# Kernel tuning notes

Hardware: AMD Instinct MI355X
Metric: run time of the kernel (lower is better)

Reference implementation:

```python
import jax, jax.numpy as jnp
import numpy as np

WS = 8      # window size
SS = 4      # shift size
NH = 4      # num heads
EPS = 1e-5
MLP_RATIO = 4


def _win_part(x, ws):
    # x: [B,D,H,W,C] -> [B*nD*nH*nW, ws^3, C]
    B, D, H, W, C = x.shape
    x = x.reshape(B, D // ws, ws, H // ws, ws, W // ws, ws, C)
    x = x.transpose(0, 1, 3, 5, 2, 4, 6, 7)
    return x.reshape(-1, ws * ws * ws, C)


def _win_rev(w, ws, B, D, H, W):
    C = w.shape[-1]
    x = w.reshape(B, D // ws, H // ws, W // ws, ws, ws, ws, C)
    x = x.transpose(0, 1, 4, 2, 5, 3, 6, 7)
    return x.reshape(B, D, H, W, C)


def _ln(x, g, b):
    m = jnp.mean(x, axis=-1, keepdims=True)
    v = jnp.mean((x - m) ** 2, axis=-1, keepdims=True)
    return (x - m) / jnp.sqrt(v + EPS) * g + b


def _rel_index(ws):
    coords = np.stack(np.meshgrid(np.arange(ws), np.arange(ws), np.arange(ws), indexing='ij'))  # [3,ws,ws,ws]
    cf = coords.reshape(3, -1)                      # [3, ws^3]
    rel = (cf[:, :, None] - cf[:, None, :]).transpose(1, 2, 0) + (ws - 1)  # [N,N,3]
    return rel[..., 0] * (2 * ws - 1) ** 2 + rel[..., 1] * (2 * ws - 1) + rel[..., 2]


def _attn_mask(D, H, W, ws, ss):
    img = np.zeros((1, D, H, W, 1), dtype=np.float32)
    cnt = 0
    sl = (slice(0, -ws), slice(-ws, -ss), slice(-ss, None))
    for d in sl:
        for h in sl:
            for w in sl:
                img[:, d, h, w, :] = cnt
                cnt += 1
    mw = np.asarray(_win_part(jnp.asarray(img), ws))[..., 0]  # [nW, ws^3]
    diff = mw[:, None, :] - mw[:, :, None]
    return np.where(diff != 0, -100.0, 0.0).astype(np.float32)


def setup_inputs() -> dict:
    key = jax.random.key(0)
    ks = jax.random.split(key, 12)
    B, D, H, W, C = 1, 16, 64, 64, 128
    mh = MLP_RATIO * C
    s = 0.02
    return {
        'x': jax.random.normal(ks[0], (B, D, H, W, C), jnp.float32),
        'attn_mask': jnp.asarray(_attn_mask(D, H, W, WS, SS)),
        'rel_index': jnp.asarray(_rel_index(WS), jnp.int32),
        'rel_bias': jax.random.normal(ks[1], ((2 * WS - 1) ** 3, NH), jnp.float32) * s,
        'qkv_w': jax.random.normal(ks[2], (3 * C, C), jnp.float32) * s,
        'qkv_b': jnp.zeros((3 * C,), jnp.float32),
        'proj_w': jax.random.normal(ks[3], (C, C), jnp.float32) * s,
        'proj_b': jnp.zeros((C,), jnp.float32),
        'norm1_g': jnp.ones((C,), jnp.float32),
        'norm1_b': jnp.zeros((C,), jnp.float32),
        'norm2_g': jnp.ones((C,), jnp.float32),
        'norm2_b': jnp.zeros((C,), jnp.float32),
        'mlp_w1': jax.random.normal(ks[4], (mh, C), jnp.float32) * s,
        'mlp_b1': jnp.zeros((mh,), jnp.float32),
        'mlp_w2': jax.random.normal(ks[5], (C, mh), jnp.float32) * s,
        'mlp_b2': jnp.zeros((C,), jnp.float32),
    }


def reference(x, attn_mask, rel_index, rel_bias, qkv_w, qkv_b, proj_w, proj_b,
              norm1_g, norm1_b, norm2_g, norm2_b, mlp_w1, mlp_b1, mlp_w2, mlp_b2):
    B, D, H, W, C = x.shape
    ws, ss, nh = WS, SS, NH
    hd = C // nh
    scale = hd ** -0.5
    N = ws ** 3
    shortcut = x
    h = _ln(x, norm1_g, norm1_b)
    h = jnp.roll(h, (-ss, -ss, -ss), axis=(1, 2, 3))
    xw = _win_part(h, ws)                 # [B_, N, C]
    B_ = xw.shape[0]
    nW = attn_mask.shape[0]
    qkv = xw @ qkv_w.T + qkv_b            # [B_, N, 3C]
    qkv = qkv.reshape(B_, N, 3, nh, hd).transpose(2, 0, 3, 1, 4)  # [3,B_,h,N,hd]
    q, k, v = qkv[0] * scale, qkv[1], qkv[2]
    attn = jnp.einsum('bhnd,bhmd->bhnm', q, k)
    rpe = rel_bias[rel_index.reshape(-1)].reshape(N, N, nh).transpose(2, 0, 1)  # [h,N,N]
    attn = attn + rpe[None]
    attn = attn.reshape(B_ // nW, nW, nh, N, N) + attn_mask[None, :, None]
    attn = jax.nn.softmax(attn.reshape(B_, nh, N, N), axis=-1)
    out = jnp.einsum('bhnm,bhmd->bhnd', attn, v).transpose(0, 2, 1, 3).reshape(B_, N, C)
    out = out @ proj_w.T + proj_b
    out = _win_rev(out, ws, B, D, H, W)
    out = jnp.roll(out, (ss, ss, ss), axis=(1, 2, 3))
    x = shortcut + out
    h2 = _ln(x, norm2_g, norm2_b)
    h2 = jax.nn.gelu(h2 @ mlp_w1.T + mlp_b1, approximate=False)
    return x + h2 @ mlp_w2.T + mlp_b2
```

## Files before the change

kernel.cpp:

```cpp
#include <hip/hip_runtime.h>
#include <math.h>

typedef __bf16 bf16;
typedef __bf16 bf16x4 __attribute__((ext_vector_type(4)));
typedef __bf16 bf16x8 __attribute__((ext_vector_type(8)));
typedef float f32x4 __attribute__((ext_vector_type(4)));
typedef unsigned short u16;
typedef u16 u16x2 __attribute__((ext_vector_type(2)));

#define LOG2E 1.4426950408889634f

__device__ __forceinline__ float b2f(u16 b) {
  return (float)__builtin_bit_cast(bf16, b);
}

__global__ void sniff_k(const unsigned* __restrict__ xw_, int* __restrict__ flag) {
  int lane = threadIdx.x;
  int c = 0;
#pragma unroll
  for (int j = 0; j < 4; j++) {
    unsigned e = (xw_[lane * 4 + j] >> 7) & 0xFFu;
    c += (e >= 100u && e <= 140u) ? 1 : 0;
  }
#pragma unroll
  for (int d = 1; d < 64; d <<= 1) c += __shfl_xor(c, d);
  if (lane == 0) *flag = (c >= 150) ? 1 : 0;
}

__global__ __launch_bounds__(256) void canon_norm_k(
    const void* __restrict__ sg, const void* __restrict__ sb,
    bf16* __restrict__ dg, bf16* __restrict__ db, const int* __restrict__ flag) {
  int i = threadIdx.x;
  int fl = *flag;
  if (i < 128) {
    dg[i] = fl ? ((const bf16*)sg)[i] : (bf16)((const float*)sg)[i];
  } else {
    int j = i - 128;
    db[j] = fl ? ((const bf16*)sb)[j] : (bf16)((const float*)sb)[j];
  }
}

struct ProArgs {
  const int* ridx;
  const void* rbias;
  bf16* rpem;
  const void* x;
  const bf16* g1;
  const bf16* b1n;
  bf16* xw;
  const void* csrc[12];
  bf16* cdst[12];
  int cn[12];
};

__global__ __launch_bounds__(256) void pro_k(ProArgs a,
                                             const int* __restrict__ flag) {
  const int bx = blockIdx.x, tid = threadIdx.x;
  const int fl = *flag;
  if (bx < 8192) {
    int t = bx * 256 + tid;
    int m0 = (t & 127) * 4, q = (t >> 7) & 511, h = (t >> 16) & 3, ty = t >> 18;
    int qd = q >> 6, qh = (q >> 3) & 7, qw = q & 7;
    int kt = m0 >> 6, mt = (m0 >> 4) & 3, quad = (m0 >> 2) & 3;
    int4 ri = *(const int4*)&a.ridx[q * 512 + m0];
    const int rv[4] = {ri.x, ri.y, ri.z, ri.w};
    bf16x4 o;
#pragma unroll
    for (int j = 0; j < 4; j++) {
      int m = m0 + j;
      int md = m >> 6, mh = (m >> 3) & 7, mw = m & 7;
      bool diff = ((ty & 4) && ((qd < 4) != (md < 4))) ||
                  ((ty & 2) && ((qh < 4) != (mh < 4))) ||
                  ((ty & 1) && ((qw < 4) != (mw < 4)));
      float bv = fl ? (float)((const bf16*)a.rbias)[rv[j] * 4 + h]
                    : ((const float*)a.rbias)[rv[j] * 4 + h];
      float v = bv * LOG2E;
      o[j] = (bf16)(v + (diff ? -144.2695041f : 0.f));
    }
    size_t out = ((size_t)(ty * 4 + h) << 18) +
                 (((size_t)(kt * 4 + quad) * 512 + q) * 16 + mt * 4);
    *(bf16x4*)&a.rpem[out] = o;
  } else if (bx < 24576) {
    int wave = tid >> 6, lane = tid & 63;
    int tok = (bx - 8192) * 4 + wave;
    int win = tok >> 9, pos = tok & 511;
    int rd = (win >> 6) * 8 + (pos >> 6);
    int rh = ((win >> 3) & 7) * 8 + ((pos >> 3) & 7);
    int rw = (win & 7) * 8 + (pos & 7);
    int od = (rd + 4) & 15, oh = (rh + 4) & 63, ow = (rw + 4) & 63;
    size_t src = (size_t)((od * 64 + oh) * 64 + ow) * 128;
    int ch = lane * 2;
    float f0, f1;
    if (!fl) {
      const float* xf = (const float*)a.x + src + ch;
      f0 = xf[0];
      f1 = xf[1];
    } else {
      u16x2 xv = *(const u16x2*)((const bf16*)a.x + src + ch);
      f0 = b2f(xv[0]);
      f1 = b2f(xv[1]);
    }
    float s = f0 + f1, sq = f0 * f0 + f1 * f1;
#pragma unroll
    for (int d = 1; d < 64; d <<= 1) {
      s += __shfl_xor(s, d);
      sq += __shfl_xor(sq, d);
    }
    float mean = s * (1.f / 128.f);
    float var = sq * (1.f / 128.f) - mean * mean;
    float rstd = rsqrtf(fmaxf(var, 0.f) + 1e-5f);
    u16x2 gv = *(const u16x2*)(a.g1 + ch), bv = *(const u16x2*)(a.b1n + ch);
    u16x2 ov;
    ov[0] =
        __builtin_bit_cast(u16, (bf16)((f0 - mean) * rstd * b2f(gv[0]) + b2f(bv[0])));
    ov[1] =
        __builtin_bit_cast(u16, (bf16)((f1 - mean) * rstd * b2f(gv[1]) + b2f(bv[1])));
    *(u16x2*)(a.xw + (size_t)tok * 128 + ch) = ov;
  } else {
    int seg = bx - 24576;
    int ti = seg >> 8;
    int i = (seg & 255) * 256 + tid;
    if (i < a.cn[ti]) {
      if (fl)
        a.cdst[ti][i] = ((const bf16*)a.csrc[ti])[i];
      else
        a.cdst[ti][i] = (bf16)((const float*)a.csrc[ti])[i];
    }
  }
}

template <int EPI, int BM, int BK, int N_, int K_>
__global__ __launch_bounds__(256) void gemm_k(const bf16* __restrict__ A,
                                              const bf16* __restrict__ B,
                                              const bf16* __restrict__ bias,
                                              void* __restrict__ outv,
                                              const void* __restrict__ residv,
                                              const int* __restrict__ flag) {
  constexpr int NC = K_ / BK;
  constexpr int NBUF = (NC > 1) ? 2 : 1;
  __shared__ __align__(16) u16 SM[NBUF][(BM + 128) * BK];
  const int t = threadIdx.x;
  const int wave = t >> 6, lane = t & 63, l15 = lane & 15, quad = lane >> 4;
  const int m0 = blockIdx.x * BM, n0 = blockIdx.y * 128;
  constexpr int MI = BM / 32;
  int fl = 0;
  if constexpr (EPI == 1) fl = *flag;
  f32x4 acc[MI][4] = {};
  const int wr = (wave >> 1) * (BM / 2), wc = (wave & 1) * 64;
  constexpr int TPR = BK / 8;
  constexpr int RPP = 256 / TPR;
  constexpr int PASSES = (BM + 128) / RPP;
  const int srow = t / TPR, sc16 = t % TPR;

  auto stage = [&](int c, int buf) {
#pragma unroll
    for (int p = 0; p < PASSES; p++) {
      int row = p * RPP + srow;
      int cs = sc16 ^ (row & 7);
      const u16* src;
      if (row < BM)
        src = (const u16*)A + (size_t)(m0 + row) * K_ + c * BK + cs * 8;
      else
        src = (const u16*)B + (size_t)(n0 + row - BM) * K_ + c * BK + cs * 8;
      __builtin_amdgcn_global_load_lds(
          (const __attribute__((address_space(1))) void*)src,
          (__attribute__((address_space(3))) void*)&SM[buf][row * BK + sc16 * 8],
          16, 0, 0);
    }
  };

  stage(0, 0);
  __syncthreads();
#pragma unroll
  for (int c = 0; c < NC; c++) {
    if (c + 1 < NC) stage(c + 1, (c + 1) & 1);
    const char* cur = (const char*)SM[c & 1];
#pragma unroll
    for (int ks = 0; ks < BK / 32; ks++) {
      bf16x8 a[MI], b[4];
#pragma unroll
      for (int i = 0; i < MI; i++) {
        int row = wr + i * 16 + l15;
        a[i] = *(const bf16x8*)(cur + row * (BK * 2) +
                                (((ks * 4 + quad) ^ (row & 7)) << 4));
      }
#pragma unroll
      for (int j = 0; j < 4; j++) {
        int row = BM + wc + j * 16 + l15;
        b[j] = *(const bf16x8*)(cur + row * (BK * 2) +
                                (((ks * 4 + quad) ^ (row & 7)) << 4));
      }
#pragma unroll
      for (int i = 0; i < MI; i++)
#pragma unroll
        for (int j = 0; j < 4; j++)
          acc[i][j] =
              __builtin_amdgcn_mfma_f32_16x16x32_bf16(a[i], b[j], acc[i][j], 0, 0, 0);
    }
    if (c + 1 < NC) __syncthreads();
  }
  const float qscale = 0.17677669529663687f * LOG2E;
#pragma unroll
  for (int i = 0; i < MI; i++) {
#pragma unroll
    for (int r = 0; r < 4; r++) {
      int tok = m0 + wr + i * 16 + quad * 4 + r;
      size_t obase = 0;
      if constexpr (EPI == 1) {
        int win = tok >> 9, pos = tok & 511;
        int rd = (win >> 6) * 8 + (pos >> 6);
        int rh = ((win >> 3) & 7) * 8 + ((pos >> 3) & 7);
        int rw = (win & 7) * 8 + (pos & 7);
        int od = (rd + 4) & 15, oh = (rh + 4) & 63, ow = (rw + 4) & 63;
        obase = (size_t)((od * 64 + oh) * 64 + ow) * 128;
      }
#pragma unroll
      for (int j = 0; j < 4; j++) {
        int gn = n0 + wc + j * 16 + l15;
        float v = acc[i][j][r] + (float)bias[gn];
        if constexpr (EPI == 0) {
          int tensor = gn >> 7, c = gn & 127, head = c >> 5, d = c & 31;
          if (tensor == 0) v *= qscale;
          int win = tok >> 9, pos = tok & 511;
          size_t off = ((((size_t)tensor * 4 + head) * 128 + win) * 512 + pos) * 32 + d;
          ((bf16*)outv)[off] = (bf16)v;
        } else {
          float rs = fl ? (float)((const bf16*)residv)[obase + gn]
                        : ((const float*)residv)[obase + gn];
          v += rs;
          ((bf16*)outv)[obase + gn] = (bf16)v;
        }
      }
    }
  }
}

__global__ __launch_bounds__(256) void mlp_k(const bf16* __restrict__ X2,
                                             const bf16* __restrict__ G2,
                                             const bf16* __restrict__ B2n,
                                             const bf16* __restrict__ W1,
                                             const bf16* __restrict__ B1,
                                             const bf16* __restrict__ W2,
                                             const bf16* __restrict__ B2,
                                             void* __restrict__ outv,
                                             const int* __restrict__ flag) {
  __shared__ __align__(16) u16 sA[32 * 128];
  __shared__ __align__(16) u16 sB[128 * 128];
  __shared__ __align__(16) u16 sH[32 * 520];
  const int t = threadIdx.x;
  const int wave = t >> 6, lane = t & 63, l15 = lane & 15, quad = lane >> 4;
  const int m0 = blockIdx.x * 32;
  const int wr = (wave >> 1) * 16, wc = (wave & 1) * 64;
  const int fl = *flag;
  const int srow = t >> 4, sc16 = t & 15;

  auto stage_w = [&](const bf16* W, int chunk, int wK) {
#pragma unroll
    for (int p = 0; p < 8; p++) {
      int row = p * 16 + srow;
      int cs = sc16 ^ (row & 7);
      const u16* src = (const u16*)W +
                       (size_t)(wK == 128 ? (chunk * 128 + row) : row) * wK +
                       (wK == 128 ? 0 : chunk * 128) + cs * 8;
      __builtin_amdgcn_global_load_lds(
          (const __attribute__((address_space(1))) void*)src,
          (__attribute__((address_space(3))) void*)&sB[row * 128 + sc16 * 8], 16,
          0, 0);
    }
  };

  {
#pragma unroll
    for (int p = 0; p < 2; p++) {
      int row = p * 16 + srow;
      int cs = sc16 ^ (row & 7);
      __builtin_amdgcn_global_load_lds(
          (const __attribute__((address_space(1))) void*)((const u16*)X2 +
                                                          (size_t)(m0 + row) * 128 +
                                                          cs * 8),
          (__attribute__((address_space(3))) void*)&sA[row * 128 + sc16 * 8], 16,
          0, 0);
    }
  }
  stage_w(W1, 0, 128);
  __syncthreads();

  {
    int r = t >> 3, k = t & 7;
    bf16x8 c0 = *(const bf16x8*)&sA[r * 128 + (k * 2 + 0) * 8];
    bf16x8 c1 = *(const bf16x8*)&sA[r * 128 + (k * 2 + 1) * 8];
    float s = 0.f, sq = 0.f;
#pragma unroll
    for (int e = 0; e < 8; e++) {
      float f0 = (float)c0[e], f1 = (float)c1[e];
      s += f0 + f1;
      sq += f0 * f0 + f1 * f1;
    }
#pragma unroll
    for (int d = 1; d < 8; d <<= 1) {
      s += __shfl_xor(s, d);
      sq += __shfl_xor(sq, d);
    }
    float mean = s * (1.f / 128.f);
    float var = sq * (1.f / 128.f) - mean * mean;
    float rstd = rsqrtf(fmaxf(var, 0.f) + 1e-5f);
    __syncthreads();
#pragma unroll
    for (int j = 0; j < 2; j++) {
      int tc = ((k * 2 + j) ^ (r & 7)) * 8;
      bf16x8 gv = *(const bf16x8*)&G2[tc];
      bf16x8 bv = *(const bf16x8*)&B2n[tc];
      bf16x8 cv = j ? c1 : c0;
      bf16x8 ov;
#pragma unroll
      for (int e = 0; e < 8; e++)
        ov[e] = (bf16)(((float)cv[e] - mean) * rstd * (float)gv[e] + (float)bv[e]);
      *(bf16x8*)&sA[r * 128 + (k * 2 + j) * 8] = ov;
    }
  }
  __syncthreads();

#pragma unroll 1
  for (int nc = 0; nc < 4; nc++) {
    f32x4 acc1[4] = {};
#pragma unroll
    for (int ks = 0; ks < 4; ks++) {
      int arow = wr + l15;
      bf16x8 av = *(const bf16x8*)((const char*)sA + arow * 256 +
                                   (((ks * 4 + quad) ^ (arow & 7)) << 4));
      bf16x8 bv[4];
#pragma unroll
      for (int j = 0; j < 4; j++) {
        int row = wc + j * 16 + l15;
        bv[j] = *(const bf16x8*)((const char*)sB + row * 256 +
                                 (((ks * 4 + quad) ^ (row & 7)) << 4));
      }
#pragma unroll
      for (int j = 0; j < 4; j++)
        acc1[j] = __builtin_amdgcn_mfma_f32_16x16x32_bf16(av, bv[j], acc1[j], 0, 0, 0);
    }
#pragma unroll
    for (int j = 0; j < 4; j++) {
      int ncol = nc * 128 + wc + j * 16 + l15;
      float bj = (float)B1[ncol];
#pragma unroll
      for (int r = 0; r < 4; r++) {
        float v = acc1[j][r] + bj;
        float v2 = v * v;
        float u2 = v * (2.30220806f + 0.10294323f * v2);
        float e2 = exp2f(u2);
        v = v - v * __builtin_amdgcn_rcpf(e2 + 1.f);
        sH[(wr + quad * 4 + r) * 520 + ncol] = __builtin_bit_cast(u16, (bf16)v);
      }
    }
    __syncthreads();
    if (nc < 3)
      stage_w(W1, nc + 1, 128);
    else
      stage_w(W2, 0, 512);
    __syncthreads();
  }

  f32x4 acc2[4] = {};
#pragma unroll 1
  for (int kc = 0; kc < 4; kc++) {
#pragma unroll
    for (int ks = 0; ks < 4; ks++) {
      int arow = wr + l15;
      bf16x8 av = *(const bf16x8*)((const char*)sH + arow * 1040 +
                                   (kc * 128 + ks * 32 + quad * 8) * 2);
#pragma unroll
      for (int j = 0; j < 4; j++) {
        int row = wc + j * 16 + l15;
        bf16x8 bv = *(const bf16x8*)((const char*)sB + row * 256 +
                                     (((ks * 4 + quad) ^ (row & 7)) << 4));
        acc2[j] = __builtin_amdgcn_mfma_f32_16x16x32_bf16(av, bv, acc2[j], 0, 0, 0);
      }
    }
    if (kc < 3) {
      __syncthreads();
      stage_w(W2, kc + 1, 512);
      __syncthreads();
    }
  }
#pragma unroll
  for (int j = 0; j < 4; j++) {
    int gn = wc + j * 16 + l15;
    float bj = (float)B2[gn];
#pragma unroll
    for (int r = 0; r < 4; r++) {
      int tok = m0 + wr + quad * 4 + r;
      size_t off = (size_t)tok * 128 + gn;
      float v = acc2[j][r] + bj + (float)X2[off];
      if (fl)
        ((bf16*)outv)[off] = (bf16)v;
      else
        ((float*)outv)[off] = v;
    }
  }
}

__global__ __launch_bounds__(512, 4) void attn_k(const bf16* __restrict__ qkv,
                                                 const bf16* __restrict__ rpem,
                                                 bf16* __restrict__ att) {
  __shared__ __align__(16) bf16 sVt[32 * 512];
  __shared__ __align__(16) bf16 sP[8][32 * 64];
  const int t = threadIdx.x;
  const int p = blockIdx.x;
  const int win = ((p >> 6) << 3) | (p & 7);
  const int mid = (p >> 3) & 7;
  const int head = mid >> 1, qh = mid & 1;
  const int wave = t >> 6, lane = t & 63, l15 = lane & 15, quad = lane >> 4;

  const int wd = win >> 6, wh = (win >> 3) & 7, ww = win & 7;
  const int type = ((wd == 1) << 2) | ((wh == 7) << 1) | (ww == 7);

  const size_t hw32 = (size_t)512 * 32;
  const bf16* qp = qkv + ((size_t)(0 * 4 + head) * 128 + win) * hw32;
  const bf16* kp = qkv + ((size_t)(1 * 4 + head) * 128 + win) * hw32;
  const bf16* vp = qkv + ((size_t)(2 * 4 + head) * 128 + win) * hw32;
  const bf16* rpeh = rpem + ((size_t)(type * 4 + head) << 18);
  const int qbase = qh * 256 + wave * 32;

  {
    int kpi = t >> 3, dblk = (t & 7) * 4;
    char* sb = (char*)sVt;
#pragma unroll
    for (int kb = 0; kb < 4; kb++) {
      const bf16* v0 = vp + (size_t)(kb * 128 + 2 * kpi) * 32 + dblk;
      bf16x4 a = *(const bf16x4*)v0;
      bf16x4 b = *(const bf16x4*)(v0 + 32);
      int keyw = kb * 64 + kpi;
#pragma unroll
      for (int dd = 0; dd < 4; dd++) {
        int row = dblk + dd;
        unsigned wv = (unsigned)__builtin_bit_cast(u16, a[dd]) |
                      ((unsigned)__builtin_bit_cast(u16, b[dd]) << 16);
        *(unsigned*)(sb + ((row * 1024 + keyw * 4) ^ ((row & 7) << 4))) = wv;
      }
    }
  }

  bf16x8 qa[2];
#pragma unroll
  for (int nt = 0; nt < 2; nt++)
    qa[nt] = *(const bf16x8*)(qp + (size_t)(qbase + nt * 16 + l15) * 32 + quad * 8);

  bf16x8 ones;
#pragma unroll
  for (int e = 0; e < 8; e++) ones[e] = (bf16)1.0f;

  __syncthreads();

  f32x4 O[2][2] = {};
  f32x4 O2[2] = {};
  char* pw = (char*)sP[wave];
  const char* sv = (const char*)sVt;
  const int swz = (l15 & 7) << 4;

#pragma unroll 1
  for (int kt = 0; kt < 8; kt++) {
    bf16x8 kb[4];
    bf16x8 rv8[2][2];
#pragma unroll
    for (int mt = 0; mt < 4; mt++)
      kb[mt] = *(const bf16x8*)(kp + (size_t)(kt * 64 + mt * 16 + l15) * 32 +
                                quad * 8);
#pragma unroll
    for (int nt = 0; nt < 2; nt++) {
      const bf16* rb =
          rpeh + ((size_t)(kt * 4 + quad) * 512 + (qbase + nt * 16 + l15)) * 16;
      rv8[nt][0] = *(const bf16x8*)rb;
      rv8[nt][1] = *(const bf16x8*)(rb + 8);
    }
    f32x4 S[4][2];
#pragma unroll
    for (int mt = 0; mt < 4; mt++)
#pragma unroll
      for (int nt = 0; nt < 2; nt++) {
        f32x4 c;
#pragma unroll
        for (int r = 0; r < 4; r++) c[r] = (float)rv8[nt][mt >> 1][(mt & 1) * 4 + r];
        S[mt][nt] = __builtin_amdgcn_mfma_f32_16x16x32_bf16(kb[mt], qa[nt], c, 0, 0, 0);
      }
#pragma unroll
    for (int nt = 0; nt < 2; nt++)
#pragma unroll
      for (int mt = 0; mt < 4; mt++) {
        bf16x4 pv;
#pragma unroll
        for (int r = 0; r < 4; r++) pv[r] = (bf16)exp2f(S[mt][nt][r]);
        *(bf16x4*)(pw + (((nt * 16 + l15) * 128 + mt * 32 + quad * 8) ^ swz)) = pv;
      }
#pragma unroll
    for (int s = 0; s < 2; s++) {
      int vc = kt * 128 + s * 64 + quad * 16;
      int pc = s * 64 + quad * 16;
      bf16x8 va0 = *(const bf16x8*)(sv + ((l15 * 1024 + vc) ^ swz));
      bf16x8 va1 = *(const bf16x8*)(sv + (((16 + l15) * 1024 + vc) ^ swz));
      bf16x8 pb0 = *(const bf16x8*)(pw + ((l15 * 128 + pc) ^ swz));
      bf16x8 pb1 = *(const bf16x8*)(pw + (((16 + l15) * 128 + pc) ^ swz));
      O[0][0] = __builtin_amdgcn_mfma_f32_16x16x32_bf16(va0, pb0, O[0][0], 0, 0, 0);
      O[0][1] = __builtin_amdgcn_mfma_f32_16x16x32_bf16(va0, pb1, O[0][1], 0, 0, 0);
      O[1][0] = __builtin_amdgcn_mfma_f32_16x16x32_bf16(va1, pb0, O[1][0], 0, 0, 0);
      O[1][1] = __builtin_amdgcn_mfma_f32_16x16x32_bf16(va1, pb1, O[1][1], 0, 0, 0);
      O2[0] = __builtin_amdgcn_mfma_f32_16x16x32_bf16(ones, pb0, O2[0], 0, 0, 0);
      O2[1] = __builtin_amdgcn_mfma_f32_16x16x32_bf16(ones, pb1, O2[1], 0, 0, 0);
    }
  }
#pragma unroll
  for (int nt = 0; nt < 2; nt++) {
    float inv = __builtin_amdgcn_rcpf(O2[nt][0]);
    int q = qbase + nt * 16 + l15;
#pragma unroll
    for (int dm = 0; dm < 2; dm++) {
      bf16x4 o;
#pragma unroll
      for (int r = 0; r < 4; r++) o[r] = (bf16)(O[dm][nt][r] * inv);
      *(bf16x4*)(att + ((size_t)win * 512 + q) * 128 + head * 32 + dm * 16 +
                 quad * 4) = o;
    }
  }
}

extern "C" void kernel_launch(void* const* d_in, const int* in_sizes, int n_in,
                              void* d_out, int out_size, void* d_ws,
                              size_t ws_size, hipStream_t stream) {
  const int* rel_index = (const int*)d_in[2];
  char* w = (char*)d_ws;

  int* flag = (int*)w;
  bf16* qw_c = (bf16*)(w + (128ull << 10));
  bf16* pw_c = (bf16*)(w + (256ull << 10));
  bf16* w1_c = (bf16*)(w + (320ull << 10));
  bf16* w2_c = (bf16*)(w + (512ull << 10));
  bf16* qb_c = (bf16*)(w + (704ull << 10));
  bf16* pb_c = (bf16*)(w + (708ull << 10));
  bf16* g1_c = (bf16*)(w + (712ull << 10));
  bf16* b1n_c = (bf16*)(w + (716ull << 10));
  bf16* g2_c = (bf16*)(w + (720ull << 10));
  bf16* b2n_c = (bf16*)(w + (724ull << 10));
  bf16* mb1_c = (bf16*)(w + (728ull << 10));
  bf16* mb2_c = (bf16*)(w + (732ull << 10));
  bf16* xw = (bf16*)(w + (17ull << 20));
  bf16* qkvb = (bf16*)(w + (33ull << 20));
  bf16* x2 = (bf16*)(w + (99ull << 20));
  bf16* rpem = x2;
  bf16* att = xw;

  sniff_k<<<1, 64, 0, stream>>>((const unsigned*)d_in[0], flag);
  canon_norm_k<<<1, 256, 0, stream>>>(d_in[8], d_in[9], g1_c, b1n_c, flag);

  ProArgs pa;
  pa.ridx = rel_index;
  pa.rbias = d_in[3];
  pa.rpem = rpem;
  pa.x = d_in[0];
  pa.g1 = g1_c;
  pa.b1n = b1n_c;
  pa.xw = xw;
  const int srcidx[12] = {4, 5, 6, 7, 8, 9, 10, 11, 12, 13, 14, 15};
  bf16* dsts[12] = {qw_c, qb_c, pw_c, pb_c, g1_c, b1n_c,
                    g2_c, b2n_c, w1_c, mb1_c, w2_c, mb2_c};
  for (int i = 0; i < 12; i++) {
    pa.csrc[i] = d_in[srcidx[i]];
    pa.cdst[i] = dsts[i];
    pa.cn[i] = in_sizes[srcidx[i]];
  }
  pro_k<<<27648, 256, 0, stream>>>(pa, flag);

  gemm_k<0, 32, 128, 384, 128><<<dim3(2048, 3), 256, 0, stream>>>(
      xw, qw_c, qb_c, qkvb, nullptr, flag);
  attn_k<<<1024, 512, 0, stream>>>(qkvb, rpem, att);
  gemm_k<1, 32, 128, 128, 128><<<dim3(2048, 1), 256, 0, stream>>>(
      att, pw_c, pb_c, x2, d_in[0], flag);
  mlp_k<<<2048, 256, 0, stream>>>(x2, g2_c, b2n_c, w1_c, mb1_c, w2_c, mb2_c,
                                  d_out, flag);
}
```

Baseline: 376.8 us.

## Prefetch MLP weights into registers and merge attention query halves per block

In the MLP kernel, the next weight chunk is now loaded from global memory into registers before the current chunk's MFMA work and written to LDS afterwards, replacing direct global-to-LDS loads issued after the barrier. The aim is to hide weight-fetch latency behind compute, at the cost of extra VGPRs. In the attention kernel, each block now handles both query halves of a window-head in a loop, halving the grid to 512 blocks. This reuses the V tile staged in LDS across both halves but reduces parallelism.

```diff
diff --git a/kernel.cpp b/kernel.cpp
--- a/kernel.cpp
+++ b/kernel.cpp
@@ -254,21 +254,6 @@
   const int fl = *flag;
   const int srow = t >> 4, sc16 = t & 15;
 
-  auto stage_w = [&](const bf16* W, int chunk, int wK) {
-#pragma unroll
-    for (int p = 0; p < 8; p++) {
-      int row = p * 16 + srow;
-      int cs = sc16 ^ (row & 7);
-      const u16* src = (const u16*)W +
-                       (size_t)(wK == 128 ? (chunk * 128 + row) : row) * wK +
-                       (wK == 128 ? 0 : chunk * 128) + cs * 8;
-      __builtin_amdgcn_global_load_lds(
-          (const __attribute__((address_space(1))) void*)src,
-          (__attribute__((address_space(3))) void*)&sB[row * 128 + sc16 * 8], 16,
-          0, 0);
-    }
-  };
-
   {
 #pragma unroll
     for (int p = 0; p < 2; p++) {
@@ -281,8 +266,18 @@
           (__attribute__((address_space(3))) void*)&sA[row * 128 + sc16 * 8], 16,
           0, 0);
     }
-  }
-  stage_w(W1, 0, 128);
+#pragma unroll
+    for (int p = 0; p < 8; p++) {
+      int row = p * 16 + srow;
+      int cs = sc16 ^ (row & 7);
+      __builtin_amdgcn_global_load_lds(
+          (const __attribute__((address_space(1))) void*)((const u16*)W1 +
+                                                          (size_t)row * 128 +
+                                                          cs * 8),
+          (__attribute__((address_space(3))) void*)&sB[row * 128 + sc16 * 8], 16,
+          0, 0);
+    }
+  }
   __syncthreads();
 
   {
@@ -320,8 +315,24 @@
   }
   __syncthreads();
 
+  bf16x8 wreg[8];
+
 #pragma unroll 1
   for (int nc = 0; nc < 4; nc++) {
+    {
+      const bf16* Wn = (nc < 3) ? W1 : W2;
+      const int chunk = (nc < 3) ? nc + 1 : 0;
+      const int wK = (nc < 3) ? 128 : 512;
+#pragma unroll
+      for (int p = 0; p < 8; p++) {
+        int row = p * 16 + srow;
+        int cs = sc16 ^ (row & 7);
+        const u16* src = (const u16*)Wn +
+                         (size_t)(wK == 128 ? (chunk * 128 + row) : row) * wK +
+                         (wK == 128 ? 0 : chunk * 128) + cs * 8;
+        wreg[p] = *(const bf16x8*)src;
+      }
+    }
     f32x4 acc1[4] = {};
 #pragma unroll
     for (int ks = 0; ks < 4; ks++) {
@@ -354,16 +365,28 @@
       }
     }
     __syncthreads();
-    if (nc < 3)
-      stage_w(W1, nc + 1, 128);
-    else
-      stage_w(W2, 0, 512);
+#pragma unroll
+    for (int p = 0; p < 8; p++) {
+      int row = p * 16 + srow;
+      *(bf16x8*)&sB[row * 128 + sc16 * 8] = wreg[p];
+    }
     __syncthreads();
   }
 
   f32x4 acc2[4] = {};
 #pragma unroll 1
   for (int kc = 0; kc < 4; kc++) {
+    if (kc < 3) {
+      const int chunk = kc + 1;
+#pragma unroll
+      for (int p = 0; p < 8; p++) {
+        int row = p * 16 + srow;
+        int cs = sc16 ^ (row & 7);
+        const u16* src =
+            (const u16*)W2 + (size_t)row * 512 + chunk * 128 + cs * 8;
+        wreg[p] = *(const bf16x8*)src;
+      }
+    }
 #pragma unroll
     for (int ks = 0; ks < 4; ks++) {
       int arow = wr + l15;
@@ -379,7 +402,11 @@
     }
     if (kc < 3) {
       __syncthreads();
-      stage_w(W2, kc + 1, 512);
+#pragma unroll
+      for (int p = 0; p < 8; p++) {
+        int row = p * 16 + srow;
+        *(bf16x8*)&sB[row * 128 + sc16 * 8] = wreg[p];
+      }
       __syncthreads();
     }
   }
@@ -407,9 +434,8 @@
   __shared__ __align__(16) bf16 sP[8][32 * 64];
   const int t = threadIdx.x;
   const int p = blockIdx.x;
-  const int win = ((p >> 6) << 3) | (p & 7);
-  const int mid = (p >> 3) & 7;
-  const int head = mid >> 1, qh = mid & 1;
+  const int win = ((p >> 5) << 3) | (p & 7);
+  const int head = (p >> 3) & 3;
   const int wave = t >> 6, lane = t & 63, l15 = lane & 15, quad = lane >> 4;
 
   const int wd = win >> 6, wh = (win >> 3) & 7, ww = win & 7;
@@ -420,7 +446,6 @@
   const bf16* kp = qkv + ((size_t)(1 * 4 + head) * 128 + win) * hw32;
   const bf16* vp = qkv + ((size_t)(2 * 4 + head) * 128 + win) * hw32;
   const bf16* rpeh = rpem + ((size_t)(type * 4 + head) << 18);
-  const int qbase = qh * 256 + wave * 32;
 
   {
     int kpi = t >> 3, dblk = (t & 7) * 4;
@@ -441,84 +466,93 @@
     }
   }
 
-  bf16x8 qa[2];
-#pragma unroll
-  for (int nt = 0; nt < 2; nt++)
-    qa[nt] = *(const bf16x8*)(qp + (size_t)(qbase + nt * 16 + l15) * 32 + quad * 8);
-
   bf16x8 ones;
 #pragma unroll
   for (int e = 0; e < 8; e++) ones[e] = (bf16)1.0f;
 
   __syncthreads();
 
-  f32x4 O[2][2] = {};
-  f32x4 O2[2] = {};
   char* pw = (char*)sP[wave];
   const char* sv = (const char*)sVt;
   const int swz = (l15 & 7) << 4;
 
 #pragma unroll 1
-  for (int kt = 0; kt < 8; kt++) {
-    bf16x8 kb[4];
-    bf16x8 rv8[2][2];
-#pragma unroll
-    for (int mt = 0; mt < 4; mt++)
-      kb[mt] = *(const bf16x8*)(kp + (size_t)(kt * 64 + mt * 16 + l15) * 32 +
-                                quad * 8);
+  for (int qh = 0; qh < 2; qh++) {
+    const int qbase = qh * 256 + wave * 32;
+    bf16x8 qa[2];
+#pragma unroll
+    for (int nt = 0; nt < 2; nt++)
+      qa[nt] =
+          *(const bf16x8*)(qp + (size_t)(qbase + nt * 16 + l15) * 32 + quad * 8);
+
+    f32x4 O[2][2] = {};
+    f32x4 O2[2] = {};
+
+#pragma unroll 1
+    for (int kt = 0; kt < 8; kt++) {
+      bf16x8 kb[4];
+      bf16x8 rv8[2][2];
+#pragma unroll
+      for (int mt = 0; mt < 4; mt++)
+        kb[mt] = *(const bf16x8*)(kp + (size_t)(kt * 64 + mt * 16 + l15) * 32 +
+                                  quad * 8);
+#pragma unroll
+      for (int nt = 0; nt < 2; nt++) {
+        const bf16* rb =
+            rpeh + ((size_t)(kt * 4 + quad) * 512 + (qbase + nt * 16 + l15)) * 16;
+        rv8[nt][0] = *(const bf16x8*)rb;
+        rv8[nt][1] = *(const bf16x8*)(rb + 8);
+      }
+      f32x4 S[4][2];
+#pragma unroll
+      for (int mt = 0; mt < 4; mt++)
+#pragma unroll
+        for (int nt = 0; nt < 2; nt++) {
+          f32x4 c;
+#pragma unroll
+          for (int r = 0; r < 4; r++)
+            c[r] = (float)rv8[nt][mt >> 1][(mt & 1) * 4 + r];
+          S[mt][nt] =
+              __builtin_amdgcn_mfma_f32_16x16x32_bf16(kb[mt], qa[nt], c, 0, 0, 0);
+        }
+#pragma unroll
+      for (int nt = 0; nt < 2; nt++)
+#pragma unroll
+        for (int mt = 0; mt < 4; mt++) {
+          bf16x4 pv;
+#pragma unroll
+          for (int r = 0; r < 4; r++) pv[r] = (bf16)exp2f(S[mt][nt][r]);
+          *(bf16x4*)(pw + (((nt * 16 + l15) * 128 + mt * 32 + quad * 8) ^ swz)) =
+              pv;
+        }
+#pragma unroll
+      for (int s = 0; s < 2; s++) {
+        int vc = kt * 128 + s * 64 + quad * 16;
+        int pc = s * 64 + quad * 16;
+        bf16x8 va0 = *(const bf16x8*)(sv + ((l15 * 1024 + vc) ^ swz));
+        bf16x8 va1 = *(const bf16x8*)(sv + (((16 + l15) * 1024 + vc) ^ swz));
+        bf16x8 pb0 = *(const bf16x8*)(pw + ((l15 * 128 + pc) ^ swz));
+        bf16x8 pb1 = *(const bf16x8*)(pw + (((16 + l15) * 128 + pc) ^ swz));
+        O[0][0] = __builtin_amdgcn_mfma_f32_16x16x32_bf16(va0, pb0, O[0][0], 0, 0, 0);
+        O[0][1] = __builtin_amdgcn_mfma_f32_16x16x32_bf16(va0, pb1, O[0][1], 0, 0, 0);
+        O[1][0] = __builtin_amdgcn_mfma_f32_16x16x32_bf16(va1, pb0, O[1][0], 0, 0, 0);
+        O[1][1] = __builtin_amdgcn_mfma_f32_16x16x32_bf16(va1, pb1, O[1][1], 0, 0, 0);
+        O2[0] = __builtin_amdgcn_mfma_f32_16x16x32_bf16(ones, pb0, O2[0], 0, 0, 0);
+        O2[1] = __builtin_amdgcn_mfma_f32_16x16x32_bf16(ones, pb1, O2[1], 0, 0, 0);
+      }
+    }
 #pragma unroll
     for (int nt = 0; nt < 2; nt++) {
-      const bf16* rb =
-          rpeh + ((size_t)(kt * 4 + quad) * 512 + (qbase + nt * 16 + l15)) * 16;
-      rv8[nt][0] = *(const bf16x8*)rb;
-      rv8[nt][1] = *(const bf16x8*)(rb + 8);
-    }
-    f32x4 S[4][2];
-#pragma unroll
-    for (int mt = 0; mt < 4; mt++)
-#pragma unroll
-      for (int nt = 0; nt < 2; nt++) {
-        f32x4 c;
-#pragma unroll
-        for (int r = 0; r < 4; r++) c[r] = (float)rv8[nt][mt >> 1][(mt & 1) * 4 + r];
-        S[mt][nt] = __builtin_amdgcn_mfma_f32_16x16x32_bf16(kb[mt], qa[nt], c, 0, 0, 0);
-      }
-#pragma unroll
-    for (int nt = 0; nt < 2; nt++)
-#pragma unroll
-      for (int mt = 0; mt < 4; mt++) {
-        bf16x4 pv;
-#pragma unroll
-        for (int r = 0; r < 4; r++) pv[r] = (bf16)exp2f(S[mt][nt][r]);
-        *(bf16x4*)(pw + (((nt * 16 + l15) * 128 + mt * 32 + quad * 8) ^ swz)) = pv;
-      }
-#pragma unroll
-    for (int s = 0; s < 2; s++) {
-      int vc = kt * 128 + s * 64 + quad * 16;
-      int pc = s * 64 + quad * 16;
-      bf16x8 va0 = *(const bf16x8*)(sv + ((l15 * 1024 + vc) ^ swz));
-      bf16x8 va1 = *(const bf16x8*)(sv + (((16 + l15) * 1024 + vc) ^ swz));
-      bf16x8 pb0 = *(const bf16x8*)(pw + ((l15 * 128 + pc) ^ swz));
-      bf16x8 pb1 = *(const bf16x8*)(pw + (((16 + l15) * 128 + pc) ^ swz));
-      O[0][0] = __builtin_amdgcn_mfma_f32_16x16x32_bf16(va0, pb0, O[0][0], 0, 0, 0);
-      O[0][1] = __builtin_amdgcn_mfma_f32_16x16x32_bf16(va0, pb1, O[0][1], 0, 0, 0);
-      O[1][0] = __builtin_amdgcn_mfma_f32_16x16x32_bf16(va1, pb0, O[1][0], 0, 0, 0);
-      O[1][1] = __builtin_amdgcn_mfma_f32_16x16x32_bf16(va1, pb1, O[1][1], 0, 0, 0);
-      O2[0] = __builtin_amdgcn_mfma_f32_16x16x32_bf16(ones, pb0, O2[0], 0, 0, 0);
-      O2[1] = __builtin_amdgcn_mfma_f32_16x16x32_bf16(ones, pb1, O2[1], 0, 0, 0);
-    }
-  }
-#pragma unroll
-  for (int nt = 0; nt < 2; nt++) {
-    float inv = __builtin_amdgcn_rcpf(O2[nt][0]);
-    int q = qbase + nt * 16 + l15;
-#pragma unroll
-    for (int dm = 0; dm < 2; dm++) {
-      bf16x4 o;
-#pragma unroll
-      for (int r = 0; r < 4; r++) o[r] = (bf16)(O[dm][nt][r] * inv);
-      *(bf16x4*)(att + ((size_t)win * 512 + q) * 128 + head * 32 + dm * 16 +
-                 quad * 4) = o;
+      float inv = __builtin_amdgcn_rcpf(O2[nt][0]);
+      int q = qbase + nt * 16 + l15;
+#pragma unroll
+      for (int dm = 0; dm < 2; dm++) {
+        bf16x4 o;
+#pragma unroll
+        for (int r = 0; r < 4; r++) o[r] = (bf16)(O[dm][nt][r] * inv);
+        *(bf16x4*)(att + ((size_t)win * 512 + q) * 128 + head * 32 + dm * 16 +
+                   quad * 4) = o;
+      }
     }
   }
 }
@@ -571,7 +605,7 @@
 
   gemm_k<0, 32, 128, 384, 128><<<dim3(2048, 3), 256, 0, stream>>>(
       xw, qw_c, qb_c, qkvb, nullptr, flag);
-  attn_k<<<1024, 512, 0, stream>>>(qkvb, rpem, att);
+  attn_k<<<512, 512, 0, stream>>>(qkvb, rpem, att);
   gemm_k<1, 32, 128, 128, 128><<<dim3(2048, 1), 256, 0, stream>>>(
       att, pw_c, pb_c, x2, d_in[0], flag);
   mlp_k<<<2048, 256, 0, stream>>>(x2, g2_c, b2n_c, w1_c, mb1_c, w2_c, mb2_c,
```

Result: no change. 376.3 us (-0.1%).
